# Optimization experiments

Hardware: AMD Instinct MI355X
Metric: run time of the kernel (lower is better)

The kernel has to match this reference:

```python
import jax, jax.numpy as jnp
import numpy as np

NUM_CLASSES = 2047
TIME_WEIGHT = 2.0
EOS_COEF = 0.1
B, Q, N = 64, 100, 16


def _lsa(cost):
    """Jonker-Volgenant min-cost assignment for rectangular cost [R, C], R <= C.
    Returns (row_ind, col_ind) with row_ind = arange(R). Equivalent to
    scipy.optimize.linear_sum_assignment."""
    R, Cn = cost.shape
    u = np.zeros(R + 1)
    v = np.zeros(Cn + 1)
    p = np.zeros(Cn + 1, dtype=np.int64)  # p[j] = 1-based row matched to col j (0 = free)
    for i in range(1, R + 1):
        p[0] = i
        j0 = 0
        minv = np.full(Cn + 1, np.inf)
        used = np.zeros(Cn + 1, dtype=bool)
        way = np.zeros(Cn + 1, dtype=np.int64)
        while True:
            used[j0] = True
            i0 = p[j0]
            cur = cost[i0 - 1] - u[i0] - v[1:]
            free = ~used[1:]
            upd = free & (cur < minv[1:])
            minv[1:] = np.where(upd, cur, minv[1:])
            way[1:] = np.where(upd, j0, way[1:])
            j1 = int(np.argmin(np.where(free, minv[1:], np.inf))) + 1
            delta = minv[j1]
            u[p[used]] += delta
            v[used] -= delta
            minv[1:] = np.where(free, minv[1:] - delta, minv[1:])
            j0 = j1
            if p[j0] == 0:
                break
        while j0 != 0:  # augment along the alternating path
            j1 = way[j0]
            p[j0] = p[j1]
            j0 = j1
    col4row = np.zeros(R, dtype=np.int64)
    for j in range(1, Cn + 1):
        if p[j] > 0:
            col4row[p[j] - 1] = j - 1
    return np.arange(R), col4row


def _match(C):
    """C: np.ndarray [B, Q, N]. Returns (query_idx [B,N], target_idx [B,N])."""
    b, q, n = C.shape
    qs = np.zeros((b, n), np.int64)
    ts = np.zeros((b, n), np.int64)
    for i in range(b):
        r, c = _lsa(C[i].T)  # rows = targets (N), cols = queries (Q); N <= Q
        ts[i] = r
        qs[i] = c
    return qs, ts


def setup_inputs() -> dict:
    key = jax.random.key(0)
    k1, k2, k3, k4 = jax.random.split(key, 4)
    pred_logits = jax.random.normal(k1, (B, Q, NUM_CLASSES + 1), dtype=jnp.float32)
    pred_time = jax.random.uniform(k2, (B, Q, 1), dtype=jnp.float32)
    labels = jax.random.randint(k3, (B, N), 1, NUM_CLASSES + 1)  # class 0 = no-object
    timestamps = jax.random.uniform(k4, (B, N, 1), dtype=jnp.float32)
    return {"pred_logits": pred_logits, "pred_time": pred_time,
            "labels": labels, "timestamps": timestamps}


def reference(pred_logits, pred_time, labels, timestamps):
    b, q = pred_logits.shape[:2]
    n = labels.shape[1]
    # --- Hungarian matching cost (detached, host-side assignment as in the original) ---
    probs = jax.nn.softmax(pred_logits, axis=-1)                              # [B,Q,C+1]
    cost_class = -jnp.take_along_axis(probs, labels[:, None, :], axis=2)      # [B,Q,N]
    cost_time = jnp.abs(pred_time[..., 0][:, :, None] -
                        timestamps[..., 0][:, None, :])                       # [B,Q,N] (cdist p=1)
    C = cost_class + TIME_WEIGHT * cost_time
    Cnp = np.nan_to_num(np.asarray(jax.device_get(C)),
                        nan=100.0, posinf=100.0, neginf=-100.0)
    qs, ts = _match(Cnp)
    qs_j = jnp.asarray(qs)  # matched query indices  [B,N]
    ts_j = jnp.asarray(ts)  # matched target indices [B,N]
    # --- weighted cross entropy over all queries ---
    class_ids = jnp.take_along_axis(labels, ts_j, axis=1)                     # [B,N]
    batch_ar = jnp.arange(b)[:, None]
    target_classes = jnp.zeros((b, q), dtype=jnp.int64).at[batch_ar, qs_j].set(class_ids)
    logZ = jax.nn.logsumexp(pred_logits, axis=-1)                             # [B,Q]
    tgt_logit = jnp.take_along_axis(pred_logits, target_classes[..., None], axis=2)[..., 0]
    nll = logZ - tgt_logit                                                    # [B,Q]
    ce_w = jnp.ones(NUM_CLASSES + 1, jnp.float32).at[0].set(EOS_COEF)
    w = ce_w[target_classes]
    loss_ce = jnp.sum(w * nll) / jnp.sum(w)
    # --- L1 loss on matched timestamps ---
    matched_pred = pred_time[batch_ar, qs_j, 0]                               # [B,N]
    matched_tgt = jnp.take_along_axis(timestamps[..., 0], ts_j, axis=1)       # [B,N]
    loss_time = jnp.mean(jnp.abs(matched_pred - matched_tgt))
    return loss_ce + TIME_WEIGHT * loss_time
```

## Files before the change

### kernel.cpp

```cpp
#include <hip/hip_runtime.h>
#include <hip/hip_bf16.h>
#include <math.h>

#define BB 64
#define QQ 100
#define NN 16
#define CC 2048
#define TIME_WEIGHT 2.0f
#define EOS_COEF 0.1f

__global__ __launch_bounds__(256) void lse_cost_kernel(
    const float* __restrict__ logits, const float* __restrict__ ptime,
    const int* __restrict__ labels, const float* __restrict__ tstamp,
    float* __restrict__ logZ, float* __restrict__ Cg,
    float* __restrict__ lsepart)
{
    const int wave = threadIdx.x >> 6;
    const int lane = threadIdx.x & 63;
    const int bq = blockIdx.x * 4 + wave;
    const int b = bq / QQ, q = bq % QQ;
    const float4* row4 = (const float4*)(logits + (size_t)bq * CC);

    float4 v[8];
    #pragma unroll
    for (int c = 0; c < 8; ++c) v[c] = row4[c * 64 + lane];

    float m = -INFINITY;
    #pragma unroll
    for (int c = 0; c < 8; ++c)
        m = fmaxf(m, fmaxf(fmaxf(v[c].x, v[c].y), fmaxf(v[c].z, v[c].w)));
    #pragma unroll
    for (int s = 1; s < 64; s <<= 1) m = fmaxf(m, __shfl_xor(m, s, 64));

    float sum = 0.f;
    #pragma unroll
    for (int c = 0; c < 8; ++c)
        sum += expf(v[c].x - m) + expf(v[c].y - m) +
               expf(v[c].z - m) + expf(v[c].w - m);
    #pragma unroll
    for (int s = 1; s < 64; s <<= 1) sum += __shfl_xor(sum, s, 64);

    const float lz = m + logf(sum);
    if (lane == 0) logZ[bq] = lz;

    const float pt = ptime[bq];
    if (lane < NN) {
        int lab = labels[b * NN + lane];
        float lg = logits[(size_t)bq * CC + lab];
        float cc = -expf(lg - lz);
        float ct = fabsf(pt - tstamp[b * NN + lane]);
        float val = cc + TIME_WEIGHT * ct;
        if (isnan(val)) val = 100.0f;
        else if (isinf(val)) val = (val > 0.f) ? 100.0f : -100.0f;
        Cg[((size_t)b * NN + lane) * QQ + q] = val;
    }

    __shared__ float red[4];
    if (lane == 0) red[wave] = lz - logits[(size_t)bq * CC];
    __syncthreads();
    if (threadIdx.x == 0)
        lsepart[blockIdx.x] = red[0] + red[1] + red[2] + red[3];
}

__global__ __launch_bounds__(64) void hungarian_kernel(
    const float* __restrict__ Cg, const float* __restrict__ logits,
    const float* __restrict__ ptime, const int* __restrict__ labels,
    const float* __restrict__ tstamp, const float* __restrict__ logZ,
    float* __restrict__ cpart, float* __restrict__ tpart)
{
    const int b = blockIdx.x;
    const int t = threadIdx.x;

    __shared__ double cost[NN][QQ];
    __shared__ double u[NN + 1];
    __shared__ int p[QQ + 1];
    __shared__ int way[QQ + 1];
    __shared__ int qsl[NN];

    for (int idx = t; idx < NN * QQ; idx += 64)
        cost[idx / QQ][idx % QQ] = (double)Cg[(size_t)b * NN * QQ + idx];
    for (int idx = t; idx <= QQ; idx += 64) p[idx] = 0;
    if (t <= NN) u[t] = 0.0;

    const int jc0 = t + 1;
    const int jc1 = t + 65;
    const bool has2 = (jc1 <= QQ);
    double v0 = 0.0, v1 = 0.0;
    const double INF = __builtin_inf();

    __syncthreads();

    for (int i = 1; i <= NN; ++i) {
        double minv0 = INF, minv1 = INF;
        bool used0 = false, used1 = false;
        if (t == 0) p[0] = i;
        int j0 = 0;
        __syncthreads();

        while (true) {
            if (j0 == jc0) used0 = true;
            if (j0 == jc1) used1 = true;
            int i0 = p[j0];
            double ui0 = u[i0];

            double bestv = INF;
            int bestj = 0x7FFFFFFF;
            if (!used0) {
                double cur = cost[i0 - 1][jc0 - 1] - ui0 - v0;
                if (cur < minv0) { minv0 = cur; way[jc0] = j0; }
                bestv = minv0; bestj = jc0;
            }
            if (has2 && !used1) {
                double cur = cost[i0 - 1][jc1 - 1] - ui0 - v1;
                if (cur < minv1) { minv1 = cur; way[jc1] = j0; }
                if (minv1 < bestv) { bestv = minv1; bestj = jc1; }
            }
            #pragma unroll
            for (int s = 1; s < 64; s <<= 1) {
                double ov = __shfl_xor(bestv, s, 64);
                int oj = __shfl_xor(bestj, s, 64);
                if (ov < bestv || (ov == bestv && oj < bestj)) { bestv = ov; bestj = oj; }
            }
            double delta = bestv;
            int j1 = bestj;

            __syncthreads();

            if (t == 0) u[p[0]] += delta;
            if (used0) { u[p[jc0]] += delta; v0 -= delta; } else { minv0 -= delta; }
            if (has2) {
                if (used1) { u[p[jc1]] += delta; v1 -= delta; } else { minv1 -= delta; }
            }
            j0 = j1;
            __syncthreads();
            if (p[j0] == 0) break;
        }

        if (t == 0) {
            int jj = j0;
            while (jj != 0) {
                int jn = way[jj];
                p[jj] = p[jn];
                jj = jn;
            }
        }
        __syncthreads();
    }

    for (int idx = t + 1; idx <= QQ; idx += 64) {
        int r = p[idx];
        if (r > 0) qsl[r - 1] = idx - 1;
    }
    __syncthreads();

    float corr = 0.f, tl = 0.f;
    if (t < NN) {
        int qcol = qsl[t];
        int lab = labels[b * NN + t];
        int bq = b * QQ + qcol;
        float lz = logZ[bq];
        float lgm = logits[(size_t)bq * CC + lab];
        float lg0 = logits[(size_t)bq * CC];
        corr = (lz - lgm) - EOS_COEF * (lz - lg0);
        tl = fabsf(ptime[bq] - tstamp[b * NN + t]);
    }
    #pragma unroll
    for (int s = 1; s < 64; s <<= 1) {
        corr += __shfl_xor(corr, s, 64);
        tl   += __shfl_xor(tl, s, 64);
    }
    if (t == 0) { cpart[b] = corr; tpart[b] = tl; }
}

__global__ __launch_bounds__(256) void fin_kernel(
    const float* __restrict__ lsepart, const float* __restrict__ cpart,
    const float* __restrict__ tpart, float* __restrict__ out)
{
    const int t = threadIdx.x;
    float a0 = 0.f;
    for (int i = t; i < 1600; i += 256) a0 += lsepart[i];
    float a1 = (t < BB) ? cpart[t] : 0.f;
    float a2 = (t < BB) ? tpart[t] : 0.f;
    __shared__ float r0[256], r1[256], r2[256];
    r0[t] = a0; r1[t] = a1; r2[t] = a2;
    __syncthreads();
    for (int s = 128; s > 0; s >>= 1) {
        if (t < s) { r0[t] += r0[t + s]; r1[t] += r1[t + s]; r2[t] += r2[t + s]; }
        __syncthreads();
    }
    if (t == 0) {
        const float sum_w = (float)(BB * NN) * 1.0f
                          + (float)(BB * (QQ - NN)) * EOS_COEF;
        float loss_ce = (EOS_COEF * r0[0] + r1[0]) / sum_w;
        float loss_t  = r2[0] / (float)(BB * NN);
        out[0] = loss_ce + TIME_WEIGHT * loss_t;
    }
}

extern "C" void kernel_launch(void* const* d_in, const int* in_sizes, int n_in,
                              void* d_out, int out_size, void* d_ws, size_t ws_size,
                              hipStream_t stream) {
    const float* logits = (const float*)d_in[0];
    const float* ptime  = (const float*)d_in[1];
    const int*   labels = (const int*)d_in[2];
    const float* tstamp = (const float*)d_in[3];
    float* out = (float*)d_out;

    char* ws = (char*)d_ws;
    float* logZ    = (float*)ws;
    float* Cg      = (float*)(ws + 25600);
    float* lsepart = (float*)(ws + 435200);
    float* cpart   = (float*)(ws + 441600);
    float* tpart   = (float*)(ws + 441856);

    lse_cost_kernel<<<1600, 256, 0, stream>>>(logits, ptime, labels, tstamp,
                                              logZ, Cg, lsepart);
    hungarian_kernel<<<BB, 64, 0, stream>>>(Cg, logits, ptime, labels, tstamp,
                                            logZ, cpart, tpart);
    fin_kernel<<<1, 256, 0, stream>>>(lsepart, cpart, tpart, out);
}
```

Baseline: 124.9 us.

## Keep Hungarian state in registers with wave shuffles; fuse final reduction via atomics

The Hungarian solver's u, p and way arrays move from shared memory into per-lane registers. They are read with wave-wide __shfl, which removes the per-iteration __syncthreads barriers and the serial single-thread augmentation walk. The separate final reduction kernel is replaced by atomic accumulation plus a last-block-done counter inside the Hungarian kernel, saving one launch. This adds atomics and threadfence ordering, and the counter must be reset each call; the first kernel does that reset.

```diff
diff --git a/kernel.cpp b/kernel.cpp
--- a/kernel.cpp
+++ b/kernel.cpp
@@ -13,8 +13,11 @@
     const float* __restrict__ logits, const float* __restrict__ ptime,
     const int* __restrict__ labels, const float* __restrict__ tstamp,
     float* __restrict__ logZ, float* __restrict__ Cg,
-    float* __restrict__ lsepart)
+    float* __restrict__ lsepart, float* __restrict__ sums, int* __restrict__ counter)
 {
+    if (blockIdx.x == 0 && threadIdx.x == 0) {
+        sums[0] = 0.f; sums[1] = 0.f; *counter = 0;
+    }
     const int wave = threadIdx.x >> 6;
     const int lane = threadIdx.x & 63;
     const int bq = blockIdx.x * 4 + wave;
@@ -66,53 +69,52 @@
     const float* __restrict__ Cg, const float* __restrict__ logits,
     const float* __restrict__ ptime, const int* __restrict__ labels,
     const float* __restrict__ tstamp, const float* __restrict__ logZ,
-    float* __restrict__ cpart, float* __restrict__ tpart)
+    const float* __restrict__ lsepart, float* __restrict__ sums,
+    int* __restrict__ counter, float* __restrict__ out)
 {
     const int b = blockIdx.x;
     const int t = threadIdx.x;
 
-    __shared__ double cost[NN][QQ];
-    __shared__ double u[NN + 1];
-    __shared__ int p[QQ + 1];
-    __shared__ int way[QQ + 1];
+    __shared__ double cost[NN * QQ];
     __shared__ int qsl[NN];
 
     for (int idx = t; idx < NN * QQ; idx += 64)
-        cost[idx / QQ][idx % QQ] = (double)Cg[(size_t)b * NN * QQ + idx];
-    for (int idx = t; idx <= QQ; idx += 64) p[idx] = 0;
-    if (t <= NN) u[t] = 0.0;
+        cost[idx] = (double)Cg[(size_t)b * NN * QQ + idx];
+    __syncthreads();
 
     const int jc0 = t + 1;
     const int jc1 = t + 65;
     const bool has2 = (jc1 <= QQ);
     double v0 = 0.0, v1 = 0.0;
+    double ureg = 0.0;
+    int preg0 = 0, preg1 = 0;
     const double INF = __builtin_inf();
-
-    __syncthreads();
 
     for (int i = 1; i <= NN; ++i) {
         double minv0 = INF, minv1 = INF;
         bool used0 = false, used1 = false;
-        if (t == 0) p[0] = i;
+        int way0 = 0, way1 = 0;
+        bool inTree = (t == i - 1);
         int j0 = 0;
-        __syncthreads();
+        int i0 = i;
 
         while (true) {
-            if (j0 == jc0) used0 = true;
-            if (j0 == jc1) used1 = true;
-            int i0 = p[j0];
-            double ui0 = u[i0];
+            used0 |= (j0 == jc0);
+            used1 |= (j0 == jc1);
+            inTree = inTree || (t == i0 - 1);
+            const double u_i0 = __shfl(ureg, i0 - 1, 64);
+            const double* crow = &cost[(i0 - 1) * QQ];
 
             double bestv = INF;
             int bestj = 0x7FFFFFFF;
             if (!used0) {
-                double cur = cost[i0 - 1][jc0 - 1] - ui0 - v0;
-                if (cur < minv0) { minv0 = cur; way[jc0] = j0; }
+                double cur = crow[jc0 - 1] - u_i0 - v0;
+                if (cur < minv0) { minv0 = cur; way0 = j0; }
                 bestv = minv0; bestj = jc0;
             }
             if (has2 && !used1) {
-                double cur = cost[i0 - 1][jc1 - 1] - ui0 - v1;
-                if (cur < minv1) { minv1 = cur; way[jc1] = j0; }
+                double cur = crow[jc1 - 1] - u_i0 - v1;
+                if (cur < minv1) { minv1 = cur; way1 = j0; }
                 if (minv1 < bestv) { bestv = minv1; bestj = jc1; }
             }
             #pragma unroll
@@ -121,36 +123,40 @@
                 int oj = __shfl_xor(bestj, s, 64);
                 if (ov < bestv || (ov == bestv && oj < bestj)) { bestv = ov; bestj = oj; }
             }
-            double delta = bestv;
-            int j1 = bestj;
-
-            __syncthreads();
-
-            if (t == 0) u[p[0]] += delta;
-            if (used0) { u[p[jc0]] += delta; v0 -= delta; } else { minv0 -= delta; }
-            if (has2) {
-                if (used1) { u[p[jc1]] += delta; v1 -= delta; } else { minv1 -= delta; }
-            }
+            const double delta = bestv;
+            const int j1 = bestj;
+
+            if (inTree) ureg += delta;
+            if (used0) v0 -= delta; else minv0 -= delta;
+            if (has2) { if (used1) v1 -= delta; else minv1 -= delta; }
+
             j0 = j1;
-            __syncthreads();
-            if (p[j0] == 0) break;
+            int psrc = (j0 <= 64) ? preg0 : preg1;
+            int plane = (j0 <= 64) ? (j0 - 1) : (j0 - 65);
+            int pj = __shfl(psrc, plane, 64);
+            if (pj == 0) break;
+            i0 = pj;
         }
 
-        if (t == 0) {
-            int jj = j0;
-            while (jj != 0) {
-                int jn = way[jj];
-                p[jj] = p[jn];
-                jj = jn;
-            }
+        while (j0 != 0) {
+            int wsrc = (j0 <= 64) ? way0 : way1;
+            int wlane = (j0 <= 64) ? (j0 - 1) : (j0 - 65);
+            int jn = __shfl(wsrc, wlane, 64);
+            int pv;
+            if (jn == 0) pv = i;
+            else {
+                int psrc = (jn <= 64) ? preg0 : preg1;
+                int plane = (jn <= 64) ? (jn - 1) : (jn - 65);
+                pv = __shfl(psrc, plane, 64);
+            }
+            if (j0 == jc0) preg0 = pv;
+            if (has2 && j0 == jc1) preg1 = pv;
+            j0 = jn;
         }
-        __syncthreads();
-    }
-
-    for (int idx = t + 1; idx <= QQ; idx += 64) {
-        int r = p[idx];
-        if (r > 0) qsl[r - 1] = idx - 1;
-    }
+    }
+
+    if (preg0 > 0) qsl[preg0 - 1] = jc0 - 1;
+    if (has2 && preg1 > 0) qsl[preg1 - 1] = jc1 - 1;
     __syncthreads();
 
     float corr = 0.f, tl = 0.f;
@@ -169,31 +175,31 @@
         corr += __shfl_xor(corr, s, 64);
         tl   += __shfl_xor(tl, s, 64);
     }
-    if (t == 0) { cpart[b] = corr; tpart[b] = tl; }
-}
-
-__global__ __launch_bounds__(256) void fin_kernel(
-    const float* __restrict__ lsepart, const float* __restrict__ cpart,
-    const float* __restrict__ tpart, float* __restrict__ out)
-{
-    const int t = threadIdx.x;
-    float a0 = 0.f;
-    for (int i = t; i < 1600; i += 256) a0 += lsepart[i];
-    float a1 = (t < BB) ? cpart[t] : 0.f;
-    float a2 = (t < BB) ? tpart[t] : 0.f;
-    __shared__ float r0[256], r1[256], r2[256];
-    r0[t] = a0; r1[t] = a1; r2[t] = a2;
-    __syncthreads();
-    for (int s = 128; s > 0; s >>= 1) {
-        if (t < s) { r0[t] += r0[t + s]; r1[t] += r1[t + s]; r2[t] += r2[t + s]; }
-        __syncthreads();
-    }
+
+    int old = 0;
     if (t == 0) {
-        const float sum_w = (float)(BB * NN) * 1.0f
-                          + (float)(BB * (QQ - NN)) * EOS_COEF;
-        float loss_ce = (EOS_COEF * r0[0] + r1[0]) / sum_w;
-        float loss_t  = r2[0] / (float)(BB * NN);
-        out[0] = loss_ce + TIME_WEIGHT * loss_t;
+        atomicAdd(&sums[0], corr);
+        atomicAdd(&sums[1], tl);
+        __threadfence();
+        old = atomicAdd(counter, 1);
+    }
+    old = __shfl(old, 0, 64);
+    if (old == BB - 1) {
+        __threadfence();
+        float r0 = 0.f;
+        #pragma unroll
+        for (int k = 0; k < 25; ++k) r0 += lsepart[t + 64 * k];
+        #pragma unroll
+        for (int s = 1; s < 64; s <<= 1) r0 += __shfl_xor(r0, s, 64);
+        if (t == 0) {
+            float s0 = atomicAdd(&sums[0], 0.0f);
+            float s1 = atomicAdd(&sums[1], 0.0f);
+            const float sum_w = (float)(BB * NN) * 1.0f
+                              + (float)(BB * (QQ - NN)) * EOS_COEF;
+            float loss_ce = (EOS_COEF * r0 + s0) / sum_w;
+            float loss_t  = s1 / (float)(BB * NN);
+            out[0] = loss_ce + TIME_WEIGHT * loss_t;
+        }
     }
 }
 
@@ -210,12 +216,11 @@
     float* logZ    = (float*)ws;
     float* Cg      = (float*)(ws + 25600);
     float* lsepart = (float*)(ws + 435200);
-    float* cpart   = (float*)(ws + 441600);
-    float* tpart   = (float*)(ws + 441856);
+    float* sums    = (float*)(ws + 441600);
+    int*   counter = (int*)(ws + 441608);
 
     lse_cost_kernel<<<1600, 256, 0, stream>>>(logits, ptime, labels, tstamp,
-                                              logZ, Cg, lsepart);
+                                              logZ, Cg, lsepart, sums, counter);
     hungarian_kernel<<<BB, 64, 0, stream>>>(Cg, logits, ptime, labels, tstamp,
-                                            logZ, cpart, tpart);
-    fin_kernel<<<1, 256, 0, stream>>>(lsepart, cpart, tpart, out);
+                                            logZ, lsepart, sums, counter, out);
 }
```

After: 123.3 us. Within noise of the previous version (-1.3%).
